# Kernel optimization log

Measured on AMD Instinct MI355X. Metric: run time of the kernel, lower is better.

## Reference

```python
import jax, jax.numpy as jnp
import numpy as np

DIM = 1024
NUM_HEADS = 16
DIM_PROJ = int(2 / 3 * 4 * DIM // 8 * 8)  # 2728, per source
EPS = 1e-5


def rms_norm(x, g):
    # NOTE: source computes sqrt(mean(x^2)) then divides by (rms + eps)
    rms = jnp.sqrt(jnp.mean(x * x, axis=-1, keepdims=True))
    return x / (rms + EPS) * g


def alibi_slopes(num_heads):
    base = (2.0 ** 8) ** (1.0 / num_heads)
    return jnp.asarray([1.0 / base ** (i + 1) for i in range(num_heads)], dtype=jnp.float32)


def setup_inputs() -> dict:
    key = jax.random.key(0)
    ks = jax.random.split(key, 7)
    B, T, C, P = 2, 2048, DIM, DIM_PROJ
    s = 0.02
    return {
        "x": jax.random.normal(ks[0], (B, T, C), dtype=jnp.float32),
        "g1": jnp.ones((C,), dtype=jnp.float32),
        "w_qkv": jax.random.normal(ks[1], (C, 3 * C), dtype=jnp.float32) * s,
        "w_o": jax.random.normal(ks[2], (C, C), dtype=jnp.float32) * s,
        "g2": jnp.ones((C,), dtype=jnp.float32),
        "W": jax.random.normal(ks[3], (C, P), dtype=jnp.float32) * s,
        "V": jax.random.normal(ks[4], (C, P), dtype=jnp.float32) * s,
        "W2": jax.random.normal(ks[5], (P, C), dtype=jnp.float32) * s,
    }


def reference(x, g1, w_qkv, w_o, g2, W, V, W2):
    B, T, C = x.shape
    H = NUM_HEADS
    Dh = C // H

    # --- attention sublayer ---
    h = rms_norm(x, g1)
    qkv = h @ w_qkv                              # [B,T,3C]
    q, k, v = jnp.split(qkv, 3, axis=-1)
    q = q.reshape(B, T, H, Dh).transpose(0, 2, 1, 3)  # [B,H,T,Dh]
    k = k.reshape(B, T, H, Dh).transpose(0, 2, 1, 3)
    v = v.reshape(B, T, H, Dh).transpose(0, 2, 1, 3)

    wei = jnp.einsum('bhqd,bhkd->bhqk', q, k)
    pos = jnp.arange(T)
    rel = (pos[None, :] - pos[:, None]).astype(jnp.float32)  # [T,T]
    m = alibi_slopes(H)[:, None, None]                        # [H,1,1]
    scale = C ** 0.5                                          # sqrt(dim), per source
    scores = wei / scale + m * rel
    causal = pos[None, :] <= pos[:, None]                     # [T,T]
    scores = jnp.where(causal[None, None], scores, -jnp.inf)
    attn = jax.nn.softmax(scores, axis=-1)

    out = jnp.einsum('bhqk,bhkd->bhqd', attn, v)
    concat = out.transpose(0, 2, 1, 3).reshape(B, T, C)
    x = concat @ w_o + x

    # --- SwiGLU sublayer ---
    h = rms_norm(x, g2)
    gated = jax.nn.silu(h @ W) * (h @ V)
    return gated @ W2 + x
```

## Files before the change

kernel.cpp:

```cpp
#include <hip/hip_runtime.h>
#include <math.h>

typedef __attribute__((ext_vector_type(8))) short bf16x8;
typedef __attribute__((ext_vector_type(4))) float f32x4;
typedef __attribute__((ext_vector_type(16))) float f32x16;

static __device__ __forceinline__ short f2bf(float x){
  union { float f; unsigned u; } a; a.f = x;
  unsigned r = a.u + 0x7fffu + ((a.u >> 16) & 1u);
  return (short)(r >> 16);
}

static __device__ __forceinline__ unsigned cvtpk(float lo, float hi){
  unsigned r; asm("v_cvt_pk_bf16_f32 %0, %1, %2" : "=v"(r) : "v"(lo), "v"(hi)); return r;
}

__global__ __launch_bounds__(256) void transpose_bf16_kernel(
    const float* __restrict__ in, short* __restrict__ out,
    int IR, int IC, int OR, int OC)
{
  __shared__ float tile[32][33];
  int i0 = blockIdx.x * 32;
  int j0 = blockIdx.y * 32;
  int tx = threadIdx.x, ty = threadIdx.y;
  #pragma unroll
  for (int r = 0; r < 32; r += 8){
    int j = j0 + ty + r, i = i0 + tx;
    tile[ty + r][tx] = (j < IR && i < IC) ? in[(size_t)j * IC + i] : 0.f;
  }
  __syncthreads();
  #pragma unroll
  for (int r = 0; r < 32; r += 8){
    int oi = i0 + ty + r, oj = j0 + tx;
    if (oi < OR && oj < OC) out[(size_t)oi * OC + oj] = f2bf(tile[tx][ty + r]);
  }
}

__global__ __launch_bounds__(256) void transpose_bb_kernel(
    const short* __restrict__ in, short* __restrict__ out)
{
  __shared__ short tile[32][33];
  int bh = blockIdx.z;
  int t0 = blockIdx.x * 32;
  int d0 = blockIdx.y * 32;
  int tx = threadIdx.x, ty = threadIdx.y;
  const short* src = in + ((size_t)bh * 2048 + t0) * 64 + d0;
  #pragma unroll
  for (int r = 0; r < 32; r += 8)
    tile[ty + r][tx] = src[(size_t)(ty + r) * 64 + tx];
  __syncthreads();
  short* dst = out + ((size_t)bh * 64 + d0) * 2048 + t0;
  #pragma unroll
  for (int r = 0; r < 32; r += 8)
    dst[(size_t)(ty + r) * 2048 + tx] = tile[tx][ty + r];
}

__global__ __launch_bounds__(256) void rmsnorm_kernel(
    const float* __restrict__ x, const float* __restrict__ g, short* __restrict__ out)
{
  int row = blockIdx.x, tid = threadIdx.x;
  const float4* xr = (const float4*)(x + (size_t)row * 1024);
  float4 v = xr[tid];
  float ss = v.x*v.x + v.y*v.y + v.z*v.z + v.w*v.w;
  #pragma unroll
  for (int m = 1; m < 64; m <<= 1) ss += __shfl_xor(ss, m, 64);
  __shared__ float sm[4];
  if ((tid & 63) == 0) sm[tid >> 6] = ss;
  __syncthreads();
  float tot = sm[0] + sm[1] + sm[2] + sm[3];
  float inv = 1.f / (sqrtf(tot * (1.f/1024.f)) + 1e-5f);
  float4 gv = ((const float4*)g)[tid];
  short4 o;
  o.x = f2bf(v.x * inv * gv.x);
  o.y = f2bf(v.y * inv * gv.y);
  o.z = f2bf(v.z * inv * gv.z);
  o.w = f2bf(v.w * inv * gv.w);
  *(short4*)(out + (size_t)row * 1024 + tid * 4) = o;
}

enum { EPI_F32 = 0, EPI_RESID = 1, EPI_QKV = 2, EPI_GATED = 3 };

template<int BM, int BN>
static __device__ __forceinline__ void dp_issue(
    const short* __restrict__ A, const short* __restrict__ Bt,
    short* __restrict__ lbuf, int K, int m0, int n0, int k0,
    int wave, int lane, int l)
{
  int g = (l * 8 + wave) * 64 + lane;
  const short* src;
  if (g < BM * 8){
    int row = g >> 3, cc = g & 7;
    src = A + (size_t)(m0 + row) * K + k0 + ((cc ^ (row & 7)) << 3);
  } else {
    int gb = g - BM * 8;
    int row = gb >> 3, cc = gb & 7;
    src = Bt + (size_t)(n0 + row) * K + k0 + ((cc ^ (row & 7)) << 3);
  }
  __builtin_amdgcn_global_load_lds((const __attribute__((address_space(1))) void*)src,
                                   (__attribute__((address_space(3))) void*)(lbuf + (size_t)g * 8),
                                   16, 0, 0);
}

template<int BM, int BN, int EPI>
__global__ __launch_bounds__(512, 2) void gemm_dp_kernel(
    const short* __restrict__ A, const short* __restrict__ Bt,
    int M, int N, int K,
    float* __restrict__ outF, short* __restrict__ outB,
    const float* __restrict__ resid, const float* __restrict__ Gprev,
    short* __restrict__ qb, short* __restrict__ kb, short* __restrict__ vb)
{
  constexpr int L  = (BM + BN) / 64;
  constexpr int WM = BM / 2, WN = BN / 4;
  constexpr int FR = WM / 16, FC = WN / 16;
  __shared__ short lds[2][(BM + BN) * 64];
  const int tid = threadIdx.x, lane = tid & 63, wave = tid >> 6;
  const int wr = wave >> 2, wc = wave & 3;
  const int la = lane & 15, lg = lane >> 4;

  int nbn = N / BN;
  int nwg = (M / BM) * nbn;
  int bid = blockIdx.x;
  int wg = ((nwg & 7) == 0) ? ((bid & 7) * (nwg >> 3) + (bid >> 3)) : bid;
  int m0 = (wg / nbn) * BM, n0 = (wg % nbn) * BN;

  f32x4 acc[FR][FC];
  #pragma unroll
  for (int i = 0; i < FR; ++i)
    #pragma unroll
    for (int j = 0; j < FC; ++j) acc[i][j] = f32x4{0.f, 0.f, 0.f, 0.f};

  const int NT = K >> 6;

  #pragma unroll
  for (int l = 0; l < L; ++l) dp_issue<BM, BN>(A, Bt, lds[0], K, m0, n0, 0,  wave, lane, l);
  #pragma unroll
  for (int l = 0; l < L; ++l) dp_issue<BM, BN>(A, Bt, lds[1], K, m0, n0, 64, wave, lane, l);

  for (int t = 0; t < NT; ++t){
    short* curb = lds[t & 1];
    if (t + 1 < NT){
      if constexpr (L == 8)      asm volatile("s_waitcnt vmcnt(8)" ::: "memory");
      else if constexpr (L == 6) asm volatile("s_waitcnt vmcnt(6)" ::: "memory");
      else                       asm volatile("s_waitcnt vmcnt(4)" ::: "memory");
    } else {
      asm volatile("s_waitcnt vmcnt(0)" ::: "memory");
    }
    __builtin_amdgcn_s_barrier();
    __builtin_amdgcn_sched_barrier(0);

    #pragma unroll
    for (int qr = 0; qr < FR / 4; ++qr){
      #pragma unroll
      for (int qc = 0; qc < FC / 2; ++qc){
        bf16x8 af[4][2], bfv[2][2];
        #pragma unroll
        for (int ii = 0; ii < 4; ++ii){
          int r = wr * WM + (qr * 4 + ii) * 16 + la;
          #pragma unroll
          for (int ks = 0; ks < 2; ++ks)
            af[ii][ks] = *(const bf16x8*)(curb + r * 64 + (((ks * 4 + lg) ^ (r & 7)) << 3));
        }
        #pragma unroll
        for (int jc = 0; jc < 2; ++jc){
          int rb = wc * WN + (qc * 2 + jc) * 16 + la;
          #pragma unroll
          for (int ks = 0; ks < 2; ++ks)
            bfv[jc][ks] = *(const bf16x8*)(curb + BM * 64 + rb * 64 + (((ks * 4 + lg) ^ (rb & 7)) << 3));
        }
        __builtin_amdgcn_s_setprio(1);
        #pragma unroll
        for (int ii = 0; ii < 4; ++ii)
          #pragma unroll
          for (int jc = 0; jc < 2; ++jc){
            acc[qr*4+ii][qc*2+jc] = __builtin_amdgcn_mfma_f32_16x16x32_bf16(
                af[ii][0], bfv[jc][0], acc[qr*4+ii][qc*2+jc], 0, 0, 0);
            acc[qr*4+ii][qc*2+jc] = __builtin_amdgcn_mfma_f32_16x16x32_bf16(
                af[ii][1], bfv[jc][1], acc[qr*4+ii][qc*2+jc], 0, 0, 0);
          }
        __builtin_amdgcn_s_setprio(0);
      }
    }
    __builtin_amdgcn_sched_barrier(0);
    __builtin_amdgcn_s_barrier();
    __builtin_amdgcn_sched_barrier(0);
    if (t + 2 < NT){
      #pragma unroll
      for (int l = 0; l < L; ++l)
        dp_issue<BM, BN>(A, Bt, curb, K, m0, n0, (t + 2) << 6, wave, lane, l);
    }
  }

  #pragma unroll
  for (int i = 0; i < FR; ++i){
    #pragma unroll
    for (int j = 0; j < FC; ++j){
      #pragma unroll
      for (int rr = 0; rr < 4; ++rr){
        int row = m0 + wr * WM + i * 16 + lg * 4 + rr;
        int col = n0 + wc * WN + j * 16 + la;
        float v = acc[i][j][rr];
        size_t idx = (size_t)row * N + col;
        if (EPI == EPI_F32){
          outF[idx] = v;
        } else if (EPI == EPI_RESID){
          outF[idx] = v + resid[idx];
        } else if (EPI == EPI_GATED){
          float gg = Gprev[idx];
          float s = gg / (1.f + __expf(-gg));
          outB[idx] = f2bf(s * v);
        } else {
          int which = col >> 10;
          int hh = (col & 1023) >> 6;
          int d = col & 63;
          int bb = row >> 11, tt = row & 2047;
          size_t o = (((size_t)(bb * 16 + hh) * 2048) + tt) * 64 + d;
          if (which == 0)      qb[o] = f2bf(v * 0.045084220f);
          else if (which == 1) kb[o] = f2bf(v);
          else                 vb[o] = f2bf(v);
        }
      }
    }
  }
}


#define CBASE(r) ((float)(((r) & 3) + 8 * ((r) >> 2)))
#define CBI(r)   ((((r) & 3) + 8 * ((r) >> 2)))

#define KVLOAD(KF, VF, T_)                                                      \
  do {                                                                          \
    _Pragma("unroll")                                                           \
    for (int ks = 0; ks < 4; ++ks)                                              \
      KF[ks] = *(const bf16x8*)(Kg + ((size_t)((T_) * 32 + q32)) * 64 + ks * 16 + hi * 8); \
    _Pragma("unroll")                                                           \
    for (int dk = 0; dk < 4; ++dk)                                              \
      VF[dk] = *(const bf16x8*)(Vt + ((size_t)((dk >> 1) * 32 + q32)) * 2048 + (T_) * 32 + (dk & 1) * 16 + hi * 8); \
  } while (0)

#define PROC(CK, CV, T_, DOPF, NK, NV)                                          \
  do {                                                                          \
    f32x16 sS;                                                                  \
    _Pragma("unroll") for (int i = 0; i < 16; ++i) sS[i] = 0.f;                 \
    sS = __builtin_amdgcn_mfma_f32_32x32x16_bf16(CK[0], qf[0], sS, 0, 0, 0);    \
    sS = __builtin_amdgcn_mfma_f32_32x32x16_bf16(CK[1], qf[1], sS, 0, 0, 0);    \
    sS = __builtin_amdgcn_mfma_f32_32x32x16_bf16(CK[2], qf[2], sS, 0, 0, 0);    \
    sS = __builtin_amdgcn_mfma_f32_32x32x16_bf16(CK[3], qf[3], sS, 0, 0, 0);    \
    if (DOPF) KVLOAD(NK, NV, (T_) + 2);                                         \
    float bb2 = slope2 * (float)((T_) * 32 + 4 * hi - qpos);                    \
    float sc[16];                                                               \
    _Pragma("unroll")                                                           \
    for (int r = 0; r < 16; ++r) sc[r] = (sS[r] + bb2) + slope2 * CBASE(r);     \
    if ((T_) == j){                                                             \
      _Pragma("unroll")                                                         \
      for (int r = 0; r < 16; ++r)                                              \
        sc[r] = (CBI(r) + 4 * hi <= q32) ? sc[r] : -1e30f;                      \
    }                                                                           \
    float t8[8], t4[4];                                                         \
    _Pragma("unroll") for (int i = 0; i < 8; ++i) t8[i] = fmaxf(sc[i], sc[i + 8]); \
    _Pragma("unroll") for (int i = 0; i < 4; ++i) t4[i] = fmaxf(t8[i], t8[i + 4]); \
    float mx = fmaxf(fmaxf(t4[0], t4[1]), fmaxf(t4[2], t4[3]));                 \
    mx = fmaxf(mx, __shfl_xor(mx, 32, 64));                                     \
    if (!__all(mx <= m_run + 8.f)){                                             \
      float mnew = fmaxf(m_run, mx);                                            \
      float aL = exp2f(m_run - mnew);                                           \
      l_run *= aL;                                                              \
      m_run = mnew;                                                             \
      _Pragma("unroll")                                                         \
      for (int r = 0; r < 16; ++r){                                             \
        float aq = __shfl(aL, CBI(r) + 4 * hi, 64);                             \
        o0[r] *= aq; o1[r] *= aq;                                               \
      }                                                                         \
    }                                                                           \
    float pr[16];                                                               \
    _Pragma("unroll")                                                           \
    for (int r = 0; r < 16; ++r) pr[r] = exp2f(sc[r] - m_run);                  \
    _Pragma("unroll") for (int i = 0; i < 8; ++i) t8[i] = pr[i] + pr[i + 8];    \
    _Pragma("unroll") for (int i = 0; i < 4; ++i) t4[i] = t8[i] + t8[i + 4];    \
    float ps = (t4[0] + t4[1]) + (t4[2] + t4[3]);                               \
    ps += __shfl_xor(ps, 32, 64);                                               \
    l_run += ps;                                                                \
    unsigned c0 = cvtpk(pr[0], pr[1]),   c1 = cvtpk(pr[2], pr[3]);              \
    unsigned c2 = cvtpk(pr[4], pr[5]),   c3 = cvtpk(pr[6], pr[7]);              \
    unsigned c4 = cvtpk(pr[8], pr[9]),   c5 = cvtpk(pr[10], pr[11]);            \
    unsigned c6 = cvtpk(pr[12], pr[13]), c7 = cvtpk(pr[14], pr[15]);            \
    unsigned x0 = (unsigned)__shfl_xor((int)c0, 32, 64), x1 = (unsigned)__shfl_xor((int)c1, 32, 64); \
    unsigned x2 = (unsigned)__shfl_xor((int)c2, 32, 64), x3 = (unsigned)__shfl_xor((int)c3, 32, 64); \
    unsigned x4 = (unsigned)__shfl_xor((int)c4, 32, 64), x5 = (unsigned)__shfl_xor((int)c5, 32, 64); \
    unsigned x6 = (unsigned)__shfl_xor((int)c6, 32, 64), x7 = (unsigned)__shfl_xor((int)c7, 32, 64); \
    union { unsigned u[4]; bf16x8 v; } pa0u, pa1u;                              \
    pa0u.u[0] = hi ? x2 : c0;  pa0u.u[1] = hi ? x3 : c1;                        \
    pa0u.u[2] = hi ? c2 : x0;  pa0u.u[3] = hi ? c3 : x1;                        \
    pa1u.u[0] = hi ? x6 : c4;  pa1u.u[1] = hi ? x7 : c5;                        \
    pa1u.u[2] = hi ? c6 : x4;  pa1u.u[3] = hi ? c7 : x5;                        \
    o0 = __builtin_amdgcn_mfma_f32_32x32x16_bf16(pa0u.v, CV[0], o0, 0, 0, 0);   \
    o0 = __builtin_amdgcn_mfma_f32_32x32x16_bf16(pa1u.v, CV[1], o0, 0, 0, 0);   \
    o1 = __builtin_amdgcn_mfma_f32_32x32x16_bf16(pa0u.v, CV[2], o1, 0, 0, 0);   \
    o1 = __builtin_amdgcn_mfma_f32_32x32x16_bf16(pa1u.v, CV[3], o1, 0, 0, 0);   \
  } while (0)

__global__ __launch_bounds__(512) void attn_kernel(
    const short* __restrict__ qb, const short* __restrict__ kb,
    const short* __restrict__ vtb, short* __restrict__ concat)
{
  const int T = 2048;
  int id = blockIdx.x;
  int grp = id & 7;
  int p   = id >> 3;
  int wid = threadIdx.x >> 6;
  int e   = wid & 3;
  int s   = wid >> 2;
  int bh = grp * 4 + e;
  int lane = threadIdx.x & 63;
  int q32 = lane & 31;
  int hi  = lane >> 5;
  int h = bh & 15, b = bh >> 4;

  __shared__ float partLDS[4][16][64][2];
  __shared__ float mlLDS[4][64][2];

  const short* Q  = qb  + (size_t)bh * T * 64;
  const short* Kg = kb  + (size_t)bh * T * 64;
  const short* Vt = vtb + (size_t)bh * 64 * T;

  float slope2 = exp2f(-0.5f * (float)(h + 1)) * 1.44269504f;

  for (int task = 0; task < 2; ++task){
    int j = task ? (63 - p) : p;
    int q0 = j * 32;
    int qpos = q0 + q32;

    bf16x8 qf[4];
    #pragma unroll
    for (int ks = 0; ks < 4; ++ks)
      qf[ks] = *(const bf16x8*)(Q + (size_t)qpos * 64 + ks * 16 + hi * 8);

    f32x16 o0, o1;
    #pragma unroll
    for (int i = 0; i < 16; ++i){ o0[i] = 0.f; o1[i] = 0.f; }
    float m_run = -1e30f, l_run = 0.f;

    if (s <= j){
      bf16x8 kA[4], vA[4], kB[4], vB[4];
      KVLOAD(kA, vA, s);
      int t = s;
      while (1){
        PROC(kA, vA, t, (t + 2 <= j), kB, vB);
        t += 2; if (t > j) break;
        PROC(kB, vB, t, (t + 2 <= j), kA, vA);
        t += 2; if (t > j) break;
      }
    }

    if (s == 0){
      #pragma unroll
      for (int r2 = 0; r2 < 8; ++r2){
        partLDS[e][r2][lane][0]     = o0[2 * r2];
        partLDS[e][r2][lane][1]     = o0[2 * r2 + 1];
        partLDS[e][r2 + 8][lane][0] = o1[2 * r2];
        partLDS[e][r2 + 8][lane][1] = o1[2 * r2 + 1];
      }
      mlLDS[e][lane][0] = m_run;
      mlLDS[e][lane][1] = l_run;
    }
    __syncthreads();
    if (s == 1){
      float mE = mlLDS[e][lane][0];
      float lE = mlLDS[e][lane][1];
      float mS = fmaxf(mE, m_run);
      float aE = exp2f(mE - mS);
      float aO = exp2f(m_run - mS);
      float lT = aE * lE + aO * l_run;
      float linv = 1.f / lT;
      float fE = aE * linv;
      float fO = aO * linv;
      #pragma unroll
      for (int r = 0; r < 16; ++r){
        int crow = CBI(r) + 4 * hi;
        float fEr = __shfl(fE, crow, 64);
        float fOr = __shfl(fO, crow, 64);
        float oE0 = partLDS[e][r >> 1][lane][r & 1];
        float oE1 = partLDS[e][8 + (r >> 1)][lane][r & 1];
        size_t base = ((size_t)(b * 2048 + q0 + crow)) * 1024 + h * 64;
        concat[base + q32]      = f2bf(fEr * oE0 + fOr * o0[r]);
        concat[base + 32 + q32] = f2bf(fEr * oE1 + fOr * o1[r]);
      }
    }
    __syncthreads();
  }
}

extern "C" void kernel_launch(void* const* d_in, const int* in_sizes, int n_in,
                              void* d_out, int out_size, void* d_ws, size_t ws_size,
                              hipStream_t stream)
{
  (void)in_sizes; (void)n_in; (void)out_size; (void)ws_size;
  const float* x     = (const float*)d_in[0];
  const float* g1    = (const float*)d_in[1];
  const float* w_qkv = (const float*)d_in[2];
  const float* w_o   = (const float*)d_in[3];
  const float* g2    = (const float*)d_in[4];
  const float* W     = (const float*)d_in[5];
  const float* V     = (const float*)d_in[6];
  const float* W2    = (const float*)d_in[7];
  float* out = (float*)d_out;

  char* wsb = (char*)d_ws;
  size_t off = 0;
  auto alloc = [&](size_t bytes) -> void* {
    void* p = wsb + off;
    off += (bytes + 255) & ~(size_t)255;
    return p;
  };
  short* wqkvT = (short*)alloc((size_t)3072 * 1024 * 2);
  short* woT   = (short*)alloc((size_t)1024 * 1024 * 2);
  short* WT    = (short*)alloc((size_t)2816 * 1024 * 2);
  short* VT    = (short*)alloc((size_t)2816 * 1024 * 2);
  short* W2T   = (short*)alloc((size_t)1024 * 2816 * 2);
  short* h1    = (short*)alloc((size_t)4096 * 1024 * 2);
  short* qbuf  = (short*)alloc((size_t)4096 * 1024 * 2);
  short* kbuf  = (short*)alloc((size_t)4096 * 1024 * 2);
  short* vbuf  = (short*)alloc((size_t)4096 * 1024 * 2);
  short* vtbuf = (short*)alloc((size_t)4096 * 1024 * 2);
  short* conc  = (short*)alloc((size_t)4096 * 1024 * 2);
  float* x2    = (float*)alloc((size_t)4096 * 1024 * 4);
  short* h2    = (short*)alloc((size_t)4096 * 1024 * 2);
  float* G     = (float*)alloc((size_t)4096 * 2816 * 4);
  short* gated = (short*)alloc((size_t)4096 * 2816 * 2);

  dim3 tb(32, 8);
  hipLaunchKernelGGL(transpose_bf16_kernel, dim3(96, 32), tb, 0, stream, w_qkv, wqkvT, 1024, 3072, 3072, 1024);
  hipLaunchKernelGGL(transpose_bf16_kernel, dim3(32, 32), tb, 0, stream, w_o,   woT,   1024, 1024, 1024, 1024);
  hipLaunchKernelGGL(transpose_bf16_kernel, dim3(88, 32), tb, 0, stream, W,     WT,    1024, 2728, 2816, 1024);
  hipLaunchKernelGGL(transpose_bf16_kernel, dim3(88, 32), tb, 0, stream, V,     VT,    1024, 2728, 2816, 1024);
  hipLaunchKernelGGL(transpose_bf16_kernel, dim3(32, 88), tb, 0, stream, W2,    W2T,   2728, 1024, 1024, 2816);

  hipLaunchKernelGGL(rmsnorm_kernel, dim3(4096), dim3(256), 0, stream, x, g1, h1);

  hipLaunchKernelGGL((gemm_dp_kernel<256, 128, EPI_QKV>), dim3(384), dim3(512), 0, stream,
                     h1, wqkvT, 4096, 3072, 1024,
                     (float*)nullptr, (short*)nullptr, (const float*)nullptr, (const float*)nullptr,
                     qbuf, kbuf, vbuf);

  hipLaunchKernelGGL(transpose_bb_kernel, dim3(64, 2, 32), tb, 0, stream, vbuf, vtbuf);

  hipLaunchKernelGGL(attn_kernel, dim3(256), dim3(512), 0, stream, qbuf, kbuf, vtbuf, conc);

  hipLaunchKernelGGL((gemm_dp_kernel<128, 128, EPI_RESID>), dim3(256), dim3(512), 0, stream,
                     conc, woT, 4096, 1024, 1024,
                     x2, (short*)nullptr, x, (const float*)nullptr,
                     (short*)nullptr, (short*)nullptr, (short*)nullptr);

  hipLaunchKernelGGL(rmsnorm_kernel, dim3(4096), dim3(256), 0, stream, x2, g2, h2);

  hipLaunchKernelGGL((gemm_dp_kernel<256, 128, EPI_F32>), dim3(352), dim3(512), 0, stream,
                     h2, WT, 4096, 2816, 1024,
                     G, (short*)nullptr, (const float*)nullptr, (const float*)nullptr,
                     (short*)nullptr, (short*)nullptr, (short*)nullptr);

  hipLaunchKernelGGL((gemm_dp_kernel<256, 128, EPI_GATED>), dim3(352), dim3(512), 0, stream,
                     h2, VT, 4096, 2816, 1024,
                     (float*)nullptr, gated, (const float*)nullptr, G,
                     (short*)nullptr, (short*)nullptr, (short*)nullptr);

  hipLaunchKernelGGL((gemm_dp_kernel<128, 128, EPI_RESID>), dim3(256), dim3(512), 0, stream,
                     gated, W2T, 4096, 1024, 2816,
                     out, (short*)nullptr, x2, (const float*)nullptr,
                     (short*)nullptr, (short*)nullptr, (short*)nullptr);
}
```

Measured before the change: 299.5 us.

## Fuse W and V SwiGLU GEMMs into one dual-accumulator kernel

Replaces the two separate gate and value GEMMs, which wrote a 4096x2816 fp32 intermediate G and read it back, with one kernel. That kernel loads the shared activation tile once alongside both W and V tiles and applies silu(gw)*v in the epilogue. This removes the fp32 round trip through global memory and one redundant read of h2, at the cost of larger LDS use (3 tiles) and double accumulators per thread. It also retiles the QKV GEMM from 256x128 to 128x128 blocks with twice as many workgroups.

Measured after the change: 269.2 us. -10.1%, faster.

```diff
diff --git a/kernel.cpp b/kernel.cpp
--- a/kernel.cpp
+++ b/kernel.cpp
@@ -78,7 +78,7 @@
   *(short4*)(out + (size_t)row * 1024 + tid * 4) = o;
 }
 
-enum { EPI_F32 = 0, EPI_RESID = 1, EPI_QKV = 2, EPI_GATED = 3 };
+enum { EPI_F32 = 0, EPI_RESID = 1, EPI_QKV = 2 };
 
 template<int BM, int BN>
 static __device__ __forceinline__ void dp_issue(
@@ -106,7 +106,7 @@
     const short* __restrict__ A, const short* __restrict__ Bt,
     int M, int N, int K,
     float* __restrict__ outF, short* __restrict__ outB,
-    const float* __restrict__ resid, const float* __restrict__ Gprev,
+    const float* __restrict__ resid,
     short* __restrict__ qb, short* __restrict__ kb, short* __restrict__ vb)
 {
   constexpr int L  = (BM + BN) / 64;
@@ -204,10 +204,6 @@
           outF[idx] = v;
         } else if (EPI == EPI_RESID){
           outF[idx] = v + resid[idx];
-        } else if (EPI == EPI_GATED){
-          float gg = Gprev[idx];
-          float s = gg / (1.f + __expf(-gg));
-          outB[idx] = f2bf(s * v);
         } else {
           int which = col >> 10;
           int hh = (col & 1023) >> 6;
@@ -223,6 +219,122 @@
   }
 }
 
+static __device__ __forceinline__ void wv_issue(
+    const short* __restrict__ A, const short* __restrict__ Bw, const short* __restrict__ Bv,
+    short* __restrict__ lbuf, int K, int m0, int n0, int k0,
+    int wave, int lane, int l)
+{
+  int g = (l * 8 + wave) * 64 + lane;
+  const short* src;
+  if (g < 1024){
+    int row = g >> 3, cc = g & 7;
+    src = A + (size_t)(m0 + row) * K + k0 + ((cc ^ (row & 7)) << 3);
+  } else if (g < 2048){
+    int gb = g - 1024;
+    int row = gb >> 3, cc = gb & 7;
+    src = Bw + (size_t)(n0 + row) * K + k0 + ((cc ^ (row & 7)) << 3);
+  } else {
+    int gb = g - 2048;
+    int row = gb >> 3, cc = gb & 7;
+    src = Bv + (size_t)(n0 + row) * K + k0 + ((cc ^ (row & 7)) << 3);
+  }
+  __builtin_amdgcn_global_load_lds((const __attribute__((address_space(1))) void*)src,
+                                   (__attribute__((address_space(3))) void*)(lbuf + (size_t)g * 8),
+                                   16, 0, 0);
+}
+
+__global__ __launch_bounds__(512, 2) void gemm_wv_kernel(
+    const short* __restrict__ A, const short* __restrict__ Bw, const short* __restrict__ Bv,
+    int M, int N, int K, short* __restrict__ outGated)
+{
+  __shared__ short lds[2][384 * 64];
+  const int tid = threadIdx.x, lane = tid & 63, wave = tid >> 6;
+  const int wr = wave >> 2, wc = wave & 3;
+  const int la = lane & 15, lg = lane >> 4;
+
+  int nbn = N >> 7;
+  int nwg = (M >> 7) * nbn;
+  int bid = blockIdx.x;
+  int wg = ((nwg & 7) == 0) ? ((bid & 7) * (nwg >> 3) + (bid >> 3)) : bid;
+  int m0 = (wg / nbn) << 7, n0 = (wg % nbn) << 7;
+
+  f32x4 accW[4][2], accV[4][2];
+  #pragma unroll
+  for (int i = 0; i < 4; ++i)
+    #pragma unroll
+    for (int j = 0; j < 2; ++j){
+      accW[i][j] = f32x4{0.f, 0.f, 0.f, 0.f};
+      accV[i][j] = f32x4{0.f, 0.f, 0.f, 0.f};
+    }
+
+  const int NT = K >> 6;
+
+  #pragma unroll
+  for (int l = 0; l < 6; ++l) wv_issue(A, Bw, Bv, lds[0], K, m0, n0, 0,  wave, lane, l);
+  #pragma unroll
+  for (int l = 0; l < 6; ++l) wv_issue(A, Bw, Bv, lds[1], K, m0, n0, 64, wave, lane, l);
+
+  for (int t = 0; t < NT; ++t){
+    short* curb = lds[t & 1];
+    if (t + 1 < NT) asm volatile("s_waitcnt vmcnt(6)" ::: "memory");
+    else            asm volatile("s_waitcnt vmcnt(0)" ::: "memory");
+    __builtin_amdgcn_s_barrier();
+    __builtin_amdgcn_sched_barrier(0);
+
+    bf16x8 af[4][2], bw[2][2], bv[2][2];
+    #pragma unroll
+    for (int ii = 0; ii < 4; ++ii){
+      int r = wr * 64 + ii * 16 + la;
+      #pragma unroll
+      for (int ks = 0; ks < 2; ++ks)
+        af[ii][ks] = *(const bf16x8*)(curb + r * 64 + (((ks * 4 + lg) ^ (r & 7)) << 3));
+    }
+    #pragma unroll
+    for (int jc = 0; jc < 2; ++jc){
+      int rb = wc * 32 + jc * 16 + la;
+      #pragma unroll
+      for (int ks = 0; ks < 2; ++ks){
+        bw[jc][ks] = *(const bf16x8*)(curb +  8192 + rb * 64 + (((ks * 4 + lg) ^ (rb & 7)) << 3));
+        bv[jc][ks] = *(const bf16x8*)(curb + 16384 + rb * 64 + (((ks * 4 + lg) ^ (rb & 7)) << 3));
+      }
+    }
+    __builtin_amdgcn_s_setprio(1);
+    #pragma unroll
+    for (int ii = 0; ii < 4; ++ii)
+      #pragma unroll
+      for (int jc = 0; jc < 2; ++jc){
+        accW[ii][jc] = __builtin_amdgcn_mfma_f32_16x16x32_bf16(af[ii][0], bw[jc][0], accW[ii][jc], 0, 0, 0);
+        accW[ii][jc] = __builtin_amdgcn_mfma_f32_16x16x32_bf16(af[ii][1], bw[jc][1], accW[ii][jc], 0, 0, 0);
+        accV[ii][jc] = __builtin_amdgcn_mfma_f32_16x16x32_bf16(af[ii][0], bv[jc][0], accV[ii][jc], 0, 0, 0);
+        accV[ii][jc] = __builtin_amdgcn_mfma_f32_16x16x32_bf16(af[ii][1], bv[jc][1], accV[ii][jc], 0, 0, 0);
+      }
+    __builtin_amdgcn_s_setprio(0);
+    __builtin_amdgcn_sched_barrier(0);
+    __builtin_amdgcn_s_barrier();
+    __builtin_amdgcn_sched_barrier(0);
+    if (t + 2 < NT){
+      #pragma unroll
+      for (int l = 0; l < 6; ++l)
+        wv_issue(A, Bw, Bv, curb, K, m0, n0, (t + 2) << 6, wave, lane, l);
+    }
+  }
+
+  #pragma unroll
+  for (int i = 0; i < 4; ++i){
+    #pragma unroll
+    for (int j = 0; j < 2; ++j){
+      #pragma unroll
+      for (int rr = 0; rr < 4; ++rr){
+        int row = m0 + wr * 64 + i * 16 + lg * 4 + rr;
+        int col = n0 + wc * 32 + j * 16 + la;
+        float gg = accW[i][j][rr];
+        float vv = accV[i][j][rr];
+        float s = gg / (1.f + __expf(-gg));
+        outGated[(size_t)row * N + col] = f2bf(s * vv);
+      }
+    }
+  }
+}
 
 #define CBASE(r) ((float)(((r) & 3) + 8 * ((r) >> 2)))
 #define CBI(r)   ((((r) & 3) + 8 * ((r) >> 2)))
@@ -424,7 +536,6 @@
   short* conc  = (short*)alloc((size_t)4096 * 1024 * 2);
   float* x2    = (float*)alloc((size_t)4096 * 1024 * 4);
   short* h2    = (short*)alloc((size_t)4096 * 1024 * 2);
-  float* G     = (float*)alloc((size_t)4096 * 2816 * 4);
   short* gated = (short*)alloc((size_t)4096 * 2816 * 2);
 
   dim3 tb(32, 8);
@@ -436,9 +547,9 @@
 
   hipLaunchKernelGGL(rmsnorm_kernel, dim3(4096), dim3(256), 0, stream, x, g1, h1);
 
-  hipLaunchKernelGGL((gemm_dp_kernel<256, 128, EPI_QKV>), dim3(384), dim3(512), 0, stream,
+  hipLaunchKernelGGL((gemm_dp_kernel<128, 128, EPI_QKV>), dim3(768), dim3(512), 0, stream,
                      h1, wqkvT, 4096, 3072, 1024,
-                     (float*)nullptr, (short*)nullptr, (const float*)nullptr, (const float*)nullptr,
+                     (float*)nullptr, (short*)nullptr, (const float*)nullptr,
                      qbuf, kbuf, vbuf);
 
   hipLaunchKernelGGL(transpose_bb_kernel, dim3(64, 2, 32), tb, 0, stream, vbuf, vtbuf);
@@ -447,23 +558,16 @@
 
   hipLaunchKernelGGL((gemm_dp_kernel<128, 128, EPI_RESID>), dim3(256), dim3(512), 0, stream,
                      conc, woT, 4096, 1024, 1024,
-                     x2, (short*)nullptr, x, (const float*)nullptr,
+                     x2, (short*)nullptr, x,
                      (short*)nullptr, (short*)nullptr, (short*)nullptr);
 
   hipLaunchKernelGGL(rmsnorm_kernel, dim3(4096), dim3(256), 0, stream, x2, g2, h2);
 
-  hipLaunchKernelGGL((gemm_dp_kernel<256, 128, EPI_F32>), dim3(352), dim3(512), 0, stream,
-                     h2, WT, 4096, 2816, 1024,
-                     G, (short*)nullptr, (const float*)nullptr, (const float*)nullptr,
-                     (short*)nullptr, (short*)nullptr, (short*)nullptr);
-
-  hipLaunchKernelGGL((gemm_dp_kernel<256, 128, EPI_GATED>), dim3(352), dim3(512), 0, stream,
-                     h2, VT, 4096, 2816, 1024,
-                     (float*)nullptr, gated, (const float*)nullptr, G,
-                     (short*)nullptr, (short*)nullptr, (short*)nullptr);
+  hipLaunchKernelGGL(gemm_wv_kernel, dim3(704), dim3(512), 0, stream,
+                     h2, WT, VT, 4096, 2816, 1024, gated);
 
   hipLaunchKernelGGL((gemm_dp_kernel<128, 128, EPI_RESID>), dim3(256), dim3(512), 0, stream,
                      gated, W2T, 4096, 1024, 2816,
-                     out, (short*)nullptr, x2, (const float*)nullptr,
+                     out, (short*)nullptr, x2,
                      (short*)nullptr, (short*)nullptr, (short*)nullptr);
 }
```
